# Kernel optimization log

Measured on AMD Instinct MI355X. Metric: run time of the kernel, lower is better.

The kernel has to match this reference:

```python
import jax, jax.numpy as jnp
import numpy as np


def _conv1x1(w, b, x):
    # 1x1 Conv2d == channel matmul: w [O,C], x [B,C,H,W] -> [B,O,H,W]
    return jnp.einsum('oc,bchw->bohw', w, x) + b[None, :, None, None]


def setup_inputs() -> dict:
    key = jax.random.key(0)
    ks = jax.random.split(key, 9)
    C = 512
    B, H, W = 8, 32, 32
    s = 0.02
    return {
        'x': jax.random.normal(ks[0], (B, C, H, W), dtype=jnp.float32),
        'wq': jax.random.normal(ks[1], (C, C), dtype=jnp.float32) * s,
        'bq': jax.random.normal(ks[2], (C,), dtype=jnp.float32) * s,
        'wk': jax.random.normal(ks[3], (C, C), dtype=jnp.float32) * s,
        'bk': jax.random.normal(ks[4], (C,), dtype=jnp.float32) * s,
        'wv': jax.random.normal(ks[5], (C, C), dtype=jnp.float32) * s,
        'bv': jax.random.normal(ks[6], (C,), dtype=jnp.float32) * s,
        'wo': jax.random.normal(ks[7], (C, C), dtype=jnp.float32) * s,
        'bo': jax.random.normal(ks[8], (C,), dtype=jnp.float32) * s,
        'heads': 8,
    }


def reference(x, wq, bq, wk, bk, wv, bv, wo, bo, heads):
    B, C, H, W = x.shape
    N = H * W
    d = C // heads
    scale = jnp.asarray(d, x.dtype) ** 0.5

    vx = _conv1x1(wv, bv, x)                       # value(x), reused for residual
    Q = _conv1x1(wq, bq, x).reshape(B, heads, d, N)
    K = _conv1x1(wk, bk, x).reshape(B, heads, d, N)
    V = vx.reshape(B, heads, d, N)

    attn = jax.nn.softmax(jnp.einsum('bhcn,bhcm->bhnm', Q, K) / scale, axis=-1)
    attn_out = jnp.einsum('bhnm,bhcm->bhcn', attn, V).reshape(B, C, H, W)

    out = attn_out + vx                            # residual uses value(x)
    return _conv1x1(wo, bo, out)
```

## Files before the change

kernel.cpp:

```cpp
#include <hip/hip_runtime.h>
#include <cstdint>
#include <cmath>

#define B_ 8
#define C_ 512
#define N_ 1024
#define H_ 8
#define D_ 64


using u16 = unsigned short;

typedef __bf16 bf16x8 __attribute__((ext_vector_type(8)));
typedef float  f32x4  __attribute__((ext_vector_type(4)));
typedef unsigned short us8 __attribute__((ext_vector_type(8)));

#if __has_builtin(__builtin_amdgcn_exp2f)
#define EXP2(x) __builtin_amdgcn_exp2f(x)
#else
#define EXP2(x) exp2f(x)
#endif

#define QSCALE 0.1803368801111244f


__device__ __forceinline__ float b2f(u16 u) {
    return __uint_as_float(((uint32_t)u) << 16);
}
__device__ __forceinline__ u16 f2b(float f) {
    uint32_t x = __float_as_uint(f);
    return (u16)((x + 0x7fffu + ((x >> 16) & 1u)) >> 16);
}
__device__ __forceinline__ u16 f2bt(float f) {
    return (u16)(__float_as_uint(f) >> 16);
}
__device__ __forceinline__ float sf(float f) {
    return (fabsf(f) < 1e30f) ? f : 0.0f;
}
__device__ __forceinline__ u16 sf2b(float f) { return f2b(sf(f)); }

template<bool WB>
__device__ __forceinline__ us8 ldw(const void* W, size_t idx) {
    if constexpr (WB) {
        return *(const us8*)((const u16*)W + idx);
    } else {
        const float* p = (const float*)W + idx;
        float4 a = *(const float4*)p, b = *(const float4*)(p + 4);
        us8 pk;
        pk[0] = sf2b(a.x); pk[1] = sf2b(a.y); pk[2] = sf2b(a.z); pk[3] = sf2b(a.w);
        pk[4] = sf2b(b.x); pk[5] = sf2b(b.y); pk[6] = sf2b(b.z); pk[7] = sf2b(b.w);
        return pk;
    }
}


__global__ __launch_bounds__(256) void k_wconv(
    const float* __restrict__ wq, const float* __restrict__ wk,
    const float* __restrict__ wv, const float* __restrict__ wo,
    u16* __restrict__ wb) {
    int i = blockIdx.x * 256 + threadIdx.x;
    int m = i >> 16;
    int off = (i & 65535) << 2;
    const float* src = (m == 0) ? wq : (m == 1) ? wk : (m == 2) ? wv : wo;
    float4 v = *(const float4*)&src[off];
    ushort4 w;
    w.x = sf2b(v.x); w.y = sf2b(v.y); w.z = sf2b(v.z); w.w = sf2b(v.w);
    *(ushort4*)&wb[(m << 18) + off] = w;
}


__global__ __launch_bounds__(256) void k_transpose(const float* __restrict__ x,
                                                   u16* __restrict__ xt) {
    __shared__ __align__(16) u16 t[64][72];
    const int tid = threadIdx.x;
    const int nb = blockIdx.x, cb = blockIdx.y, b = blockIdx.z;
#pragma unroll
    for (int i = 0; i < 4; ++i) {
        int q = tid + i * 256;
        int row = q >> 4, cg = q & 15;
        float4 v = *(const float4*)&x[((size_t)(b * C_ + cb * 64 + row) << 10) + nb * 64 + cg * 4];
        ushort4 w;
        w.x = sf2b(v.x); w.y = sf2b(v.y); w.z = sf2b(v.z); w.w = sf2b(v.w);
        *(ushort4*)&t[row][cg * 4] = w;
    }
    __syncthreads();
#pragma unroll
    for (int i = 0; i < 4; ++i) {
        int q = tid + i * 256;
        int nrow = q >> 4, cg = q & 15;
        ushort4 w;
        w.x = t[cg * 4 + 0][nrow];
        w.y = t[cg * 4 + 1][nrow];
        w.z = t[cg * 4 + 2][nrow];
        w.w = t[cg * 4 + 3][nrow];
        *(ushort4*)&xt[((size_t)(b * N_ + nb * 64 + nrow) << 9) + cb * 64 + cg * 4] = w;
    }
}


template<bool WB>
__global__ __launch_bounds__(256) void k_proj_t(
    const u16* __restrict__ xt,
    const void* __restrict__ wq, const float* __restrict__ bq,
    const void* __restrict__ wk, const float* __restrict__ bk,
    const void* __restrict__ wv, const float* __restrict__ bv,
    u16* __restrict__ qt, u16* __restrict__ kt,
    u16* __restrict__ v,  u16* __restrict__ vxt) {
    __shared__ __align__(16) u16 lA[128 * 64];
    __shared__ __align__(16) u16 lB[128 * 64];
    const int tid = threadIdx.x;
    const int op = blockIdx.z >> 3, b = blockIdx.z & 7;
    const int n0 = blockIdx.x * 128, o0 = blockIdx.y * 128;
    const void*  W  = (op == 0) ? wq : (op == 1) ? wk : wv;
    const float* BI = (op == 0) ? bq : (op == 1) ? bk : bv;
    const u16* A = xt + ((size_t)b << 19);
    const int lane = tid & 63, wave = tid >> 6;
    const int wm = (wave >> 1) * 64, wn = (wave & 1) * 64;
    const int l15 = lane & 15, lg = lane >> 4;
    const int xs = (l15 & 7) << 3;

    f32x4 acc[4][4];
    const f32x4 vzero = {0.f, 0.f, 0.f, 0.f};
#pragma unroll
    for (int i = 0; i < 4; ++i)
#pragma unroll
        for (int j = 0; j < 4; ++j) acc[i][j] = vzero;

    us8 ra[4], rwB[4];
    auto loadk = [&](int k0) {
#pragma unroll
        for (int p = 0; p < 4; ++p) {
            int slot = p * 256 + tid;
            int row = slot >> 3, seg = slot & 7;
            ra[p] = *(const us8*)&A[(size_t)(n0 + row) * C_ + k0 + seg * 8];
            rwB[p] = ldw<WB>(W, (size_t)(o0 + row) * C_ + k0 + seg * 8);
        }
    };
    loadk(0);

    for (int k0 = 0; k0 < C_; k0 += 64) {
        __syncthreads();
#pragma unroll
        for (int p = 0; p < 4; ++p) {
            int slot = p * 256 + tid;
            int row = slot >> 3, seg = slot & 7;
            int off = row * 64 + ((seg ^ (row & 7)) << 3);
            *(us8*)&lA[off] = ra[p];
            *(us8*)&lB[off] = rwB[p];
        }
        if (k0 + 64 < C_) loadk(k0 + 64);
        __syncthreads();
#pragma unroll
        for (int kk = 0; kk < 64; kk += 32) {
            const int col = (kk + lg * 8) ^ xs;
            bf16x8 af[4], bfr[4];
#pragma unroll
            for (int i = 0; i < 4; ++i)
                af[i] = *(const bf16x8*)&lA[(wm + i * 16 + l15) * 64 + col];
#pragma unroll
            for (int j = 0; j < 4; ++j)
                bfr[j] = *(const bf16x8*)&lB[(wn + j * 16 + l15) * 64 + col];
#pragma unroll
            for (int i = 0; i < 4; ++i)
#pragma unroll
                for (int j = 0; j < 4; ++j)
                    acc[i][j] = __builtin_amdgcn_mfma_f32_16x16x32_bf16(af[i], bfr[j], acc[i][j], 0, 0, 0);
        }
    }

    if (op < 2) {
        u16* outp = (op == 0) ? qt : kt;
        const float scl = (op == 0) ? QSCALE : 1.0f;
#pragma unroll
        for (int i = 0; i < 4; ++i) {
            int nb2 = n0 + wm + i * 16 + lg * 4;
#pragma unroll
            for (int j = 0; j < 4; ++j) {
                int o = o0 + wn + j * 16 + l15;
                float bias = sf(BI[o]);
                int h = o >> 6, dl = o & 63;
                size_t base = ((size_t)b * H_ + h) << 10;
#pragma unroll
                for (int r = 0; r < 4; ++r)
                    outp[(base + nb2 + r) * D_ + dl] = f2b((acc[i][j][r] + bias) * scl);
            }
        }
    } else {
#pragma unroll
        for (int i = 0; i < 4; ++i) {
            int nb2 = n0 + wm + i * 16 + lg * 4;
#pragma unroll
            for (int j = 0; j < 4; ++j) {
                int o = o0 + wn + j * 16 + l15;
                float bias = sf(BI[o]);
                float p0 = acc[i][j][0] + bias, p1 = acc[i][j][1] + bias;
                float p2 = acc[i][j][2] + bias, p3 = acc[i][j][3] + bias;
                ushort4 pk; pk.x = f2b(p0); pk.y = f2b(p1); pk.z = f2b(p2); pk.w = f2b(p3);
                *(ushort4*)&v[((size_t)(b * C_ + o) << 10) + nb2] = pk;
                vxt[((size_t)(b * N_ + nb2 + 0) << 9) + o] = pk.x;
                vxt[((size_t)(b * N_ + nb2 + 1) << 9) + o] = pk.y;
                vxt[((size_t)(b * N_ + nb2 + 2) << 9) + o] = pk.z;
                vxt[((size_t)(b * N_ + nb2 + 3) << 9) + o] = pk.w;
            }
        }
    }
}


__global__ __launch_bounds__(256) void k_attn(
    const u16* __restrict__ qt, const u16* __restrict__ kt,
    const u16* __restrict__ v,  const u16* __restrict__ vxt,
    u16* __restrict__ rt) {
    __shared__ __align__(16) u16 lK[64 * 64];
    __shared__ __align__(16) u16 lV[64 * 64];
    __shared__ __align__(16) u16 lP[4][32 * 64];
    const int tid = threadIdx.x, lane = tid & 63, wave = tid >> 6;
    const int l15 = lane & 15, lg = lane >> 4;
    const int xs = (l15 & 7) << 3;
    const int bid = blockIdx.x;
    const int qb = bid >> 6, bh = bid & 63;
    const int b = bh >> 3, h = bh & 7;
    const size_t bh_off = (size_t)bh << 16;
    const int q0 = qb * 128;
    const int nA = wave * 32;

    bf16x8 qf[2][2];
#pragma unroll
    for (int nt = 0; nt < 2; ++nt)
#pragma unroll
        for (int k = 0; k < 2; ++k)
            qf[nt][k] = *(const bf16x8*)&qt[bh_off +
                (size_t)(q0 + nA + nt * 16 + l15) * D_ + k * 32 + lg * 8];

    us8 rk[2], rv[2];
    auto loadkv = [&](int mb) {
#pragma unroll
        for (int p = 0; p < 2; ++p) {
            int slot = p * 256 + tid;
            int row = slot >> 3, seg = slot & 7;
            rk[p] = *(const us8*)&kt[bh_off + (size_t)(mb * 64 + row) * D_ + seg * 8];
            rv[p] = *(const us8*)&v[((size_t)(b * C_ + h * 64 + row) << 10) + mb * 64 + seg * 8];
        }
    };
    loadkv(0);

    float L[2] = {0.f, 0.f};
    f32x4 oacc[2][4];
    const f32x4 vzero = {0.f, 0.f, 0.f, 0.f};
#pragma unroll
    for (int nt = 0; nt < 2; ++nt)
#pragma unroll
        for (int ct = 0; ct < 4; ++ct) oacc[nt][ct] = vzero;

    for (int mb = 0; mb < 16; ++mb) {
        __syncthreads();
#pragma unroll
        for (int p = 0; p < 2; ++p) {
            int slot = p * 256 + tid;
            int row = slot >> 3, seg = slot & 7;
            int off = row * 64 + ((seg ^ (row & 7)) << 3);
            *(us8*)&lK[off] = rk[p];
            *(us8*)&lV[off] = rv[p];
        }
        if (mb < 15) loadkv(mb + 1);
        __syncthreads();

        f32x4 s[4][2];
#pragma unroll
        for (int mt = 0; mt < 4; ++mt)
#pragma unroll
            for (int nt = 0; nt < 2; ++nt) s[mt][nt] = vzero;
#pragma unroll
        for (int k = 0; k < 2; ++k) {
            const int col = (k * 32 + lg * 8) ^ xs;
            bf16x8 aK[4];
#pragma unroll
            for (int mt = 0; mt < 4; ++mt)
                aK[mt] = *(const bf16x8*)&lK[(mt * 16 + l15) * 64 + col];
            __builtin_amdgcn_s_setprio(1);
#pragma unroll
            for (int mt = 0; mt < 4; ++mt)
#pragma unroll
                for (int nt = 0; nt < 2; ++nt)
                    s[mt][nt] = __builtin_amdgcn_mfma_f32_16x16x32_bf16(aK[mt], qf[nt][k], s[mt][nt], 0, 0, 0);
            __builtin_amdgcn_s_setprio(0);
        }

#pragma unroll
        for (int mt = 0; mt < 4; ++mt)
#pragma unroll
            for (int nt = 0; nt < 2; ++nt) {
                float p0 = EXP2(s[mt][nt][0]);
                float p1 = EXP2(s[mt][nt][1]);
                float p2 = EXP2(s[mt][nt][2]);
                float p3 = EXP2(s[mt][nt][3]);
                L[nt] += p0 + p1 + p2 + p3;
                ushort4 pk; pk.x = f2bt(p0); pk.y = f2bt(p1); pk.z = f2bt(p2); pk.w = f2bt(p3);
                *(ushort4*)&lP[wave][(nt * 16 + l15) * 64 + ((mt * 16 + lg * 4) ^ xs)] = pk;
            }

#pragma unroll
        for (int kk2 = 0; kk2 < 64; kk2 += 32) {
            const int colv = (kk2 + lg * 8) ^ xs;
            bf16x8 aP[2], bV[4];
#pragma unroll
            for (int nt = 0; nt < 2; ++nt)
                aP[nt] = *(const bf16x8*)&lP[wave][(nt * 16 + l15) * 64 + colv];
#pragma unroll
            for (int ct = 0; ct < 4; ++ct)
                bV[ct] = *(const bf16x8*)&lV[(ct * 16 + l15) * 64 + colv];
            __builtin_amdgcn_s_setprio(1);
#pragma unroll
            for (int nt = 0; nt < 2; ++nt)
#pragma unroll
                for (int ct = 0; ct < 4; ++ct)
                    oacc[nt][ct] = __builtin_amdgcn_mfma_f32_16x16x32_bf16(aP[nt], bV[ct], oacc[nt][ct], 0, 0, 0);
            __builtin_amdgcn_s_setprio(0);
        }
    }

#pragma unroll
    for (int nt = 0; nt < 2; ++nt) {
        float s2 = L[nt];
        s2 += __shfl_xor(s2, 16);
        s2 += __shfl_xor(s2, 32);
        L[nt] = s2;
    }

#pragma unroll
    for (int nt = 0; nt < 2; ++nt) {
        float inv[4];
#pragma unroll
        for (int r = 0; r < 4; ++r) inv[r] = 1.0f / __shfl(L[nt], lg * 4 + r);
#pragma unroll
        for (int ct = 0; ct < 4; ++ct) {
            int ch = h * 64 + ct * 16 + l15;
#pragma unroll
            for (int r = 0; r < 4; ++r) {
                int n = q0 + nA + nt * 16 + lg * 4 + r;
                size_t idx = ((size_t)(b * N_ + n) << 9) + ch;
                rt[idx] = f2b(oacc[nt][ct][r] * inv[r] + b2f(vxt[idx]));
            }
        }
    }
}


template<bool WB>
__global__ __launch_bounds__(256) void k_out_t(
    const u16* __restrict__ rt, const void* __restrict__ wo,
    const float* __restrict__ bo, float* __restrict__ out) {
    __shared__ __align__(16) u16 lA[128 * 64];
    __shared__ __align__(16) u16 lB[128 * 64];
    const int tid = threadIdx.x;
    const int b = blockIdx.z;
    const int n0 = blockIdx.x * 128, o0 = blockIdx.y * 128;
    const u16* Rb = rt + ((size_t)b << 19);
    const int lane = tid & 63, wave = tid >> 6;
    const int wm = (wave >> 1) * 64, wn = (wave & 1) * 64;
    const int l15 = lane & 15, lg = lane >> 4;
    const int xs = (l15 & 7) << 3;

    f32x4 acc[4][4];
    const f32x4 vzero = {0.f, 0.f, 0.f, 0.f};
#pragma unroll
    for (int i = 0; i < 4; ++i)
#pragma unroll
        for (int j = 0; j < 4; ++j) acc[i][j] = vzero;

    us8 rb[4], rwB[4];
    auto loadk = [&](int k0) {
#pragma unroll
        for (int p = 0; p < 4; ++p) {
            int slot = p * 256 + tid;
            int row = slot >> 3, seg = slot & 7;
            rwB[p] = ldw<WB>(wo, (size_t)(o0 + row) * C_ + k0 + seg * 8);
            rb[p] = *(const us8*)&Rb[(size_t)(n0 + row) * C_ + k0 + seg * 8];
        }
    };
    loadk(0);

    for (int k0 = 0; k0 < C_; k0 += 64) {
        __syncthreads();
#pragma unroll
        for (int p = 0; p < 4; ++p) {
            int slot = p * 256 + tid;
            int row = slot >> 3, seg = slot & 7;
            int off = row * 64 + ((seg ^ (row & 7)) << 3);
            *(us8*)&lA[off] = rwB[p];
            *(us8*)&lB[off] = rb[p];
        }
        if (k0 + 64 < C_) loadk(k0 + 64);
        __syncthreads();
#pragma unroll
        for (int kk = 0; kk < 64; kk += 32) {
            const int col = (kk + lg * 8) ^ xs;
            bf16x8 af[4], bfr[4];
#pragma unroll
            for (int i = 0; i < 4; ++i)
                af[i] = *(const bf16x8*)&lA[(wm + i * 16 + l15) * 64 + col];
#pragma unroll
            for (int j = 0; j < 4; ++j)
                bfr[j] = *(const bf16x8*)&lB[(wn + j * 16 + l15) * 64 + col];
#pragma unroll
            for (int i = 0; i < 4; ++i)
#pragma unroll
                for (int j = 0; j < 4; ++j)
                    acc[i][j] = __builtin_amdgcn_mfma_f32_16x16x32_bf16(af[i], bfr[j], acc[i][j], 0, 0, 0);
        }
    }

#pragma unroll
    for (int i = 0; i < 4; ++i) {
#pragma unroll
        for (int j = 0; j < 4; ++j) {
            int nn = n0 + wn + j * 16 + l15;
#pragma unroll
            for (int r = 0; r < 4; ++r) {
                int o = o0 + wm + i * 16 + lg * 4 + r;
                out[((size_t)(b * C_ + o) << 10) + nn] = acc[i][j][r] + sf(bo[o]);
            }
        }
    }
}


extern "C" void kernel_launch(void* const* d_in, const int* in_sizes, int n_in,
                              void* d_out, int out_size, void* d_ws, size_t ws_size,
                              hipStream_t stream) {
    const float* x  = (const float*)d_in[0];
    const float* wq = (const float*)d_in[1];
    const float* bq = (const float*)d_in[2];
    const float* wk = (const float*)d_in[3];
    const float* bk = (const float*)d_in[4];
    const float* wv = (const float*)d_in[5];
    const float* bv = (const float*)d_in[6];
    const float* wo = (const float*)d_in[7];
    const float* bo = (const float*)d_in[8];
    float* out = (float*)d_out;
    u16* ws = (u16*)d_ws;

    const size_t T = (size_t)B_ * C_ * N_;
    const size_t WSZ = (size_t)4 * C_ * C_;
    if (ws_size < 5 * T * sizeof(u16)) return;

    u16* xt  = ws;
    u16* qt  = ws + 1 * T;
    u16* kt  = ws + 2 * T;
    u16* vv  = ws + 3 * T;
    u16* vxt = ws + 4 * T;
    u16* rt  = xt;
    u16* wb  = ws + 5 * T;

    const bool wbfit = ws_size >= (5 * T + WSZ) * sizeof(u16);

    k_transpose<<<dim3(16, 8, 8), 256, 0, stream>>>(x, xt);
    if (wbfit) {
        k_wconv<<<dim3(1024), 256, 0, stream>>>(wq, wk, wv, wo, wb);
        k_proj_t<true><<<dim3(8, 4, 24), 256, 0, stream>>>(
            xt, wb, bq, wb + 262144, bk, wb + 524288, bv, qt, kt, vv, vxt);
    } else {
        k_proj_t<false><<<dim3(8, 4, 24), 256, 0, stream>>>(
            xt, wq, bq, wk, bk, wv, bv, qt, kt, vv, vxt);
    }
    k_attn<<<dim3(512), 256, 0, stream>>>(qt, kt, vv, vxt, rt);
    if (wbfit) {
        k_out_t<true><<<dim3(8, 4, 8), 256, 0, stream>>>(rt, wb + 786432, bo, out);
    } else {
        k_out_t<false><<<dim3(8, 4, 8), 256, 0, stream>>>(rt, wo, bo, out);
    }
}
```

Before: 76.04 us.

## Double-buffer K/V in LDS and give each wave 64 queries across two heads

The attention kernel now processes two (batch, head) pairs per block, with each wave handling 64 query rows instead of 32. The grid halves to 256 blocks. K/V tiles are double-buffered in LDS, which removes one barrier per iteration and lets the next tile's global loads overlap with compute. The cost is much more LDS (about 96KB) and many more registers (accumulators and Q fragments double), which lowers occupancy, and 256 blocks may underfill the 256 CUs.

After: 79.58 us. 1.05x slower.

```diff
diff --git a/kernel.cpp b/kernel.cpp
--- a/kernel.cpp
+++ b/kernel.cpp
@@ -211,77 +211,96 @@
     const u16* __restrict__ qt, const u16* __restrict__ kt,
     const u16* __restrict__ v,  const u16* __restrict__ vxt,
     u16* __restrict__ rt) {
-    __shared__ __align__(16) u16 lK[64 * 64];
-    __shared__ __align__(16) u16 lV[64 * 64];
-    __shared__ __align__(16) u16 lP[4][32 * 64];
+    __shared__ __align__(16) u16 lK[2][2][64 * 64];
+    __shared__ __align__(16) u16 lV[2][2][64 * 64];
+    __shared__ __align__(16) u16 lP[4][64 * 64];
     const int tid = threadIdx.x, lane = tid & 63, wave = tid >> 6;
     const int l15 = lane & 15, lg = lane >> 4;
     const int xs = (l15 & 7) << 3;
     const int bid = blockIdx.x;
-    const int qb = bid >> 6, bh = bid & 63;
-    const int b = bh >> 3, h = bh & 7;
-    const size_t bh_off = (size_t)bh << 16;
+    const int qb = bid >> 5, bhp = bid & 31;
     const int q0 = qb * 128;
-    const int nA = wave * 32;
-
-    bf16x8 qf[2][2];
-#pragma unroll
-    for (int nt = 0; nt < 2; ++nt)
+    const int wp = wave >> 1;
+    const int nA = (wave & 1) * 64;
+    const int bh_w = bhp * 2 + wp;
+    const int b_w = bh_w >> 3, h_w = bh_w & 7;
+    const size_t bhoff_w = (size_t)bh_w << 16;
+
+    const size_t kbase0 = (size_t)(bhp * 2 + 0) << 16;
+    const size_t kbase1 = (size_t)(bhp * 2 + 1) << 16;
+    const size_t vbase0 = ((size_t)(((bhp * 2 + 0) >> 3) * C_ + ((bhp * 2 + 0) & 7) * 64) << 10);
+    const size_t vbase1 = ((size_t)(((bhp * 2 + 1) >> 3) * C_ + ((bhp * 2 + 1) & 7) * 64) << 10);
+
+    bf16x8 qf[4][2];
+#pragma unroll
+    for (int nt = 0; nt < 4; ++nt)
 #pragma unroll
         for (int k = 0; k < 2; ++k)
-            qf[nt][k] = *(const bf16x8*)&qt[bh_off +
+            qf[nt][k] = *(const bf16x8*)&qt[bhoff_w +
                 (size_t)(q0 + nA + nt * 16 + l15) * D_ + k * 32 + lg * 8];
 
-    us8 rk[2], rv[2];
+    us8 rkv[8];
     auto loadkv = [&](int mb) {
 #pragma unroll
-        for (int p = 0; p < 2; ++p) {
-            int slot = p * 256 + tid;
-            int row = slot >> 3, seg = slot & 7;
-            rk[p] = *(const us8*)&kt[bh_off + (size_t)(mb * 64 + row) * D_ + seg * 8];
-            rv[p] = *(const us8*)&v[((size_t)(b * C_ + h * 64 + row) << 10) + mb * 64 + seg * 8];
+        for (int p = 0; p < 8; ++p) {
+            int half = p >> 2, tensor = (p >> 1) & 1;
+            int rr = (p & 1) * 256 + tid;
+            int row = rr >> 3, seg = rr & 7;
+            size_t src;
+            if (tensor == 0)
+                src = (half ? kbase1 : kbase0) + (size_t)(mb * 64 + row) * D_ + seg * 8;
+            else
+                src = (half ? vbase1 : vbase0) + ((size_t)row << 10) + mb * 64 + seg * 8;
+            rkv[p] = *(const us8*)&(tensor == 0 ? kt : v)[src];
         }
     };
+    auto writekv = [&](int buf) {
+#pragma unroll
+        for (int p = 0; p < 8; ++p) {
+            int half = p >> 2, tensor = (p >> 1) & 1;
+            int rr = (p & 1) * 256 + tid;
+            int row = rr >> 3, seg = rr & 7;
+            int off = row * 64 + ((seg ^ (row & 7)) << 3);
+            if (tensor == 0) *(us8*)&lK[half][buf][off] = rkv[p];
+            else             *(us8*)&lV[half][buf][off] = rkv[p];
+        }
+    };
+
     loadkv(0);
-
-    float L[2] = {0.f, 0.f};
-    f32x4 oacc[2][4];
+    writekv(0);
+    loadkv(1);
+    __syncthreads();
+
+    float L[4] = {0.f, 0.f, 0.f, 0.f};
+    f32x4 oacc[4][4];
     const f32x4 vzero = {0.f, 0.f, 0.f, 0.f};
 #pragma unroll
-    for (int nt = 0; nt < 2; ++nt)
+    for (int nt = 0; nt < 4; ++nt)
 #pragma unroll
         for (int ct = 0; ct < 4; ++ct) oacc[nt][ct] = vzero;
 
     for (int mb = 0; mb < 16; ++mb) {
-        __syncthreads();
-#pragma unroll
-        for (int p = 0; p < 2; ++p) {
-            int slot = p * 256 + tid;
-            int row = slot >> 3, seg = slot & 7;
-            int off = row * 64 + ((seg ^ (row & 7)) << 3);
-            *(us8*)&lK[off] = rk[p];
-            *(us8*)&lV[off] = rv[p];
-        }
-        if (mb < 15) loadkv(mb + 1);
-        __syncthreads();
-
-        f32x4 s[4][2];
+        const int cur = mb & 1;
+        const u16* lKc = lK[wp][cur];
+        const u16* lVc = lV[wp][cur];
+
+        f32x4 s[4][4];
 #pragma unroll
         for (int mt = 0; mt < 4; ++mt)
 #pragma unroll
-            for (int nt = 0; nt < 2; ++nt) s[mt][nt] = vzero;
+            for (int nt = 0; nt < 4; ++nt) s[mt][nt] = vzero;
 #pragma unroll
         for (int k = 0; k < 2; ++k) {
             const int col = (k * 32 + lg * 8) ^ xs;
             bf16x8 aK[4];
 #pragma unroll
             for (int mt = 0; mt < 4; ++mt)
-                aK[mt] = *(const bf16x8*)&lK[(mt * 16 + l15) * 64 + col];
+                aK[mt] = *(const bf16x8*)&lKc[(mt * 16 + l15) * 64 + col];
             __builtin_amdgcn_s_setprio(1);
 #pragma unroll
             for (int mt = 0; mt < 4; ++mt)
 #pragma unroll
-                for (int nt = 0; nt < 2; ++nt)
+                for (int nt = 0; nt < 4; ++nt)
                     s[mt][nt] = __builtin_amdgcn_mfma_f32_16x16x32_bf16(aK[mt], qf[nt][k], s[mt][nt], 0, 0, 0);
             __builtin_amdgcn_s_setprio(0);
         }
@@ -289,7 +308,7 @@
 #pragma unroll
         for (int mt = 0; mt < 4; ++mt)
 #pragma unroll
-            for (int nt = 0; nt < 2; ++nt) {
+            for (int nt = 0; nt < 4; ++nt) {
                 float p0 = EXP2(s[mt][nt][0]);
                 float p1 = EXP2(s[mt][nt][1]);
                 float p2 = EXP2(s[mt][nt][2]);
@@ -302,25 +321,31 @@
 #pragma unroll
         for (int kk2 = 0; kk2 < 64; kk2 += 32) {
             const int colv = (kk2 + lg * 8) ^ xs;
-            bf16x8 aP[2], bV[4];
-#pragma unroll
-            for (int nt = 0; nt < 2; ++nt)
+            bf16x8 aP[4], bV[4];
+#pragma unroll
+            for (int nt = 0; nt < 4; ++nt)
                 aP[nt] = *(const bf16x8*)&lP[wave][(nt * 16 + l15) * 64 + colv];
 #pragma unroll
             for (int ct = 0; ct < 4; ++ct)
-                bV[ct] = *(const bf16x8*)&lV[(ct * 16 + l15) * 64 + colv];
+                bV[ct] = *(const bf16x8*)&lVc[(ct * 16 + l15) * 64 + colv];
             __builtin_amdgcn_s_setprio(1);
 #pragma unroll
-            for (int nt = 0; nt < 2; ++nt)
+            for (int nt = 0; nt < 4; ++nt)
 #pragma unroll
                 for (int ct = 0; ct < 4; ++ct)
                     oacc[nt][ct] = __builtin_amdgcn_mfma_f32_16x16x32_bf16(aP[nt], bV[ct], oacc[nt][ct], 0, 0, 0);
             __builtin_amdgcn_s_setprio(0);
         }
-    }
-
-#pragma unroll
-    for (int nt = 0; nt < 2; ++nt) {
+
+        if (mb < 15) {
+            writekv(cur ^ 1);
+            if (mb < 14) loadkv(mb + 2);
+        }
+        __syncthreads();
+    }
+
+#pragma unroll
+    for (int nt = 0; nt < 4; ++nt) {
         float s2 = L[nt];
         s2 += __shfl_xor(s2, 16);
         s2 += __shfl_xor(s2, 32);
@@ -328,17 +353,17 @@
     }
 
 #pragma unroll
-    for (int nt = 0; nt < 2; ++nt) {
+    for (int nt = 0; nt < 4; ++nt) {
         float inv[4];
 #pragma unroll
         for (int r = 0; r < 4; ++r) inv[r] = 1.0f / __shfl(L[nt], lg * 4 + r);
 #pragma unroll
         for (int ct = 0; ct < 4; ++ct) {
-            int ch = h * 64 + ct * 16 + l15;
+            int ch = h_w * 64 + ct * 16 + l15;
 #pragma unroll
             for (int r = 0; r < 4; ++r) {
                 int n = q0 + nA + nt * 16 + lg * 4 + r;
-                size_t idx = ((size_t)(b * N_ + n) << 9) + ch;
+                size_t idx = ((size_t)(b_w * N_ + n) << 9) + ch;
                 rt[idx] = f2b(oacc[nt][ct][r] * inv[r] + b2f(vxt[idx]));
             }
         }
@@ -463,7 +488,7 @@
         k_proj_t<false><<<dim3(8, 4, 24), 256, 0, stream>>>(
             xt, wq, bq, wk, bk, wv, bv, qt, kt, vv, vxt);
     }
-    k_attn<<<dim3(512), 256, 0, stream>>>(qt, kt, vv, vxt, rt);
+    k_attn<<<dim3(256), 256, 0, stream>>>(qt, kt, vv, vxt, rt);
     if (wbfit) {
         k_out_t<true><<<dim3(8, 4, 8), 256, 0, stream>>>(rt, wb + 786432, bo, out);
     } else {
```

## Merge weight conversion into transpose kernel and widen attention waves to 64 queries

Applied to the files above, without the earlier changes.

The separate weight-to-bf16 conversion launch is folded into the transpose kernel as an extra grid slice, removing one kernel launch. The attention kernel now runs two waves per block, each owning 64 query rows instead of 32, so K/V tiles staged in shared memory are reused across more MFMAs per load. This raises register pressure (larger score and accumulator arrays) and halves the threads per block, which may affect occupancy and latency hiding.

New measurement: 93.19 us. +22.5%, slower.

```diff
diff --git a/kernel.cpp b/kernel.cpp
--- a/kernel.cpp
+++ b/kernel.cpp
@@ -54,26 +54,32 @@
 }
 
 
-__global__ __launch_bounds__(256) void k_wconv(
-    const float* __restrict__ wq, const float* __restrict__ wk,
-    const float* __restrict__ wv, const float* __restrict__ wo,
-    u16* __restrict__ wb) {
-    int i = blockIdx.x * 256 + threadIdx.x;
-    int m = i >> 16;
-    int off = (i & 65535) << 2;
-    const float* src = (m == 0) ? wq : (m == 1) ? wk : (m == 2) ? wv : wo;
-    float4 v = *(const float4*)&src[off];
-    ushort4 w;
-    w.x = sf2b(v.x); w.y = sf2b(v.y); w.z = sf2b(v.z); w.w = sf2b(v.w);
-    *(ushort4*)&wb[(m << 18) + off] = w;
-}
-
-
-__global__ __launch_bounds__(256) void k_transpose(const float* __restrict__ x,
-                                                   u16* __restrict__ xt) {
-    __shared__ __align__(16) u16 t[64][72];
+__global__ __launch_bounds__(256) void k_pre(const float* __restrict__ x,
+                                             u16* __restrict__ xt,
+                                             const float* __restrict__ wq,
+                                             const float* __restrict__ wk,
+                                             const float* __restrict__ wv,
+                                             const float* __restrict__ wo,
+                                             u16* __restrict__ wb) {
     const int tid = threadIdx.x;
     const int nb = blockIdx.x, cb = blockIdx.y, b = blockIdx.z;
+    if (b == 8) {
+        if (wb == nullptr) return;
+        int base = (cb * 16 + nb) * 256 + tid;
+#pragma unroll
+        for (int i = 0; i < 8; ++i) {
+            int idx = base + i * 32768;
+            int m = idx >> 16;
+            int off = (idx & 65535) << 2;
+            const float* src = (m == 0) ? wq : (m == 1) ? wk : (m == 2) ? wv : wo;
+            float4 v = *(const float4*)&src[off];
+            ushort4 w;
+            w.x = sf2b(v.x); w.y = sf2b(v.y); w.z = sf2b(v.z); w.w = sf2b(v.w);
+            *(ushort4*)&wb[(m << 18) + off] = w;
+        }
+        return;
+    }
+    __shared__ __align__(16) u16 t[64][72];
 #pragma unroll
     for (int i = 0; i < 4; ++i) {
         int q = tid + i * 256;
@@ -207,13 +213,13 @@
 }
 
 
-__global__ __launch_bounds__(256) void k_attn(
+__global__ __launch_bounds__(128, 2) void k_attn(
     const u16* __restrict__ qt, const u16* __restrict__ kt,
     const u16* __restrict__ v,  const u16* __restrict__ vxt,
     u16* __restrict__ rt) {
     __shared__ __align__(16) u16 lK[64 * 64];
     __shared__ __align__(16) u16 lV[64 * 64];
-    __shared__ __align__(16) u16 lP[4][32 * 64];
+    __shared__ __align__(16) u16 lP[2][64 * 64];
     const int tid = threadIdx.x, lane = tid & 63, wave = tid >> 6;
     const int l15 = lane & 15, lg = lane >> 4;
     const int xs = (l15 & 7) << 3;
@@ -222,21 +228,21 @@
     const int b = bh >> 3, h = bh & 7;
     const size_t bh_off = (size_t)bh << 16;
     const int q0 = qb * 128;
-    const int nA = wave * 32;
-
-    bf16x8 qf[2][2];
-#pragma unroll
-    for (int nt = 0; nt < 2; ++nt)
+    const int nA = wave * 64;
+
+    bf16x8 qf[4][2];
+#pragma unroll
+    for (int nt = 0; nt < 4; ++nt)
 #pragma unroll
         for (int k = 0; k < 2; ++k)
             qf[nt][k] = *(const bf16x8*)&qt[bh_off +
                 (size_t)(q0 + nA + nt * 16 + l15) * D_ + k * 32 + lg * 8];
 
-    us8 rk[2], rv[2];
+    us8 rk[4], rv[4];
     auto loadkv = [&](int mb) {
 #pragma unroll
-        for (int p = 0; p < 2; ++p) {
-            int slot = p * 256 + tid;
+        for (int p = 0; p < 4; ++p) {
+            int slot = p * 128 + tid;
             int row = slot >> 3, seg = slot & 7;
             rk[p] = *(const us8*)&kt[bh_off + (size_t)(mb * 64 + row) * D_ + seg * 8];
             rv[p] = *(const us8*)&v[((size_t)(b * C_ + h * 64 + row) << 10) + mb * 64 + seg * 8];
@@ -244,19 +250,19 @@
     };
     loadkv(0);
 
-    float L[2] = {0.f, 0.f};
-    f32x4 oacc[2][4];
+    float L[4] = {0.f, 0.f, 0.f, 0.f};
+    f32x4 oacc[4][4];
     const f32x4 vzero = {0.f, 0.f, 0.f, 0.f};
 #pragma unroll
-    for (int nt = 0; nt < 2; ++nt)
+    for (int nt = 0; nt < 4; ++nt)
 #pragma unroll
         for (int ct = 0; ct < 4; ++ct) oacc[nt][ct] = vzero;
 
     for (int mb = 0; mb < 16; ++mb) {
         __syncthreads();
 #pragma unroll
-        for (int p = 0; p < 2; ++p) {
-            int slot = p * 256 + tid;
+        for (int p = 0; p < 4; ++p) {
+            int slot = p * 128 + tid;
             int row = slot >> 3, seg = slot & 7;
             int off = row * 64 + ((seg ^ (row & 7)) << 3);
             *(us8*)&lK[off] = rk[p];
@@ -265,11 +271,11 @@
         if (mb < 15) loadkv(mb + 1);
         __syncthreads();
 
-        f32x4 s[4][2];
+        f32x4 s[4][4];
 #pragma unroll
         for (int mt = 0; mt < 4; ++mt)
 #pragma unroll
-            for (int nt = 0; nt < 2; ++nt) s[mt][nt] = vzero;
+            for (int nt = 0; nt < 4; ++nt) s[mt][nt] = vzero;
 #pragma unroll
         for (int k = 0; k < 2; ++k) {
             const int col = (k * 32 + lg * 8) ^ xs;
@@ -281,7 +287,7 @@
 #pragma unroll
             for (int mt = 0; mt < 4; ++mt)
 #pragma unroll
-                for (int nt = 0; nt < 2; ++nt)
+                for (int nt = 0; nt < 4; ++nt)
                     s[mt][nt] = __builtin_amdgcn_mfma_f32_16x16x32_bf16(aK[mt], qf[nt][k], s[mt][nt], 0, 0, 0);
             __builtin_amdgcn_s_setprio(0);
         }
@@ -289,7 +295,7 @@
 #pragma unroll
         for (int mt = 0; mt < 4; ++mt)
 #pragma unroll
-            for (int nt = 0; nt < 2; ++nt) {
+            for (int nt = 0; nt < 4; ++nt) {
                 float p0 = EXP2(s[mt][nt][0]);
                 float p1 = EXP2(s[mt][nt][1]);
                 float p2 = EXP2(s[mt][nt][2]);
@@ -302,16 +308,16 @@
 #pragma unroll
         for (int kk2 = 0; kk2 < 64; kk2 += 32) {
             const int colv = (kk2 + lg * 8) ^ xs;
-            bf16x8 aP[2], bV[4];
-#pragma unroll
-            for (int nt = 0; nt < 2; ++nt)
+            bf16x8 aP[4], bV[4];
+#pragma unroll
+            for (int nt = 0; nt < 4; ++nt)
                 aP[nt] = *(const bf16x8*)&lP[wave][(nt * 16 + l15) * 64 + colv];
 #pragma unroll
             for (int ct = 0; ct < 4; ++ct)
                 bV[ct] = *(const bf16x8*)&lV[(ct * 16 + l15) * 64 + colv];
             __builtin_amdgcn_s_setprio(1);
 #pragma unroll
-            for (int nt = 0; nt < 2; ++nt)
+            for (int nt = 0; nt < 4; ++nt)
 #pragma unroll
                 for (int ct = 0; ct < 4; ++ct)
                     oacc[nt][ct] = __builtin_amdgcn_mfma_f32_16x16x32_bf16(aP[nt], bV[ct], oacc[nt][ct], 0, 0, 0);
@@ -320,7 +326,7 @@
     }
 
 #pragma unroll
-    for (int nt = 0; nt < 2; ++nt) {
+    for (int nt = 0; nt < 4; ++nt) {
         float s2 = L[nt];
         s2 += __shfl_xor(s2, 16);
         s2 += __shfl_xor(s2, 32);
@@ -328,7 +334,7 @@
     }
 
 #pragma unroll
-    for (int nt = 0; nt < 2; ++nt) {
+    for (int nt = 0; nt < 4; ++nt) {
         float inv[4];
 #pragma unroll
         for (int r = 0; r < 4; ++r) inv[r] = 1.0f / __shfl(L[nt], lg * 4 + r);
@@ -454,16 +460,16 @@
 
     const bool wbfit = ws_size >= (5 * T + WSZ) * sizeof(u16);
 
-    k_transpose<<<dim3(16, 8, 8), 256, 0, stream>>>(x, xt);
+    k_pre<<<dim3(16, 8, 9), 256, 0, stream>>>(x, xt, wq, wk, wv, wo,
+                                              wbfit ? wb : (u16*)nullptr);
     if (wbfit) {
-        k_wconv<<<dim3(1024), 256, 0, stream>>>(wq, wk, wv, wo, wb);
         k_proj_t<true><<<dim3(8, 4, 24), 256, 0, stream>>>(
             xt, wb, bq, wb + 262144, bk, wb + 524288, bv, qt, kt, vv, vxt);
     } else {
         k_proj_t<false><<<dim3(8, 4, 24), 256, 0, stream>>>(
             xt, wq, bq, wk, bk, wv, bv, qt, kt, vv, vxt);
     }
-    k_attn<<<dim3(512), 256, 0, stream>>>(qt, kt, vv, vxt, rt);
+    k_attn<<<dim3(512), 128, 0, stream>>>(qt, kt, vv, vxt, rt);
     if (wbfit) {
         k_out_t<true><<<dim3(8, 4, 8), 256, 0, stream>>>(rt, wb + 786432, bo, out);
     } else {
```
